# Optimization experiments

Hardware: AMD Instinct MI355X
Metric: run time of the kernel (lower is better)

The kernel has to match this reference:

```python
import jax, jax.numpy as jnp
import numpy as np

Z_DIM = 256
HID = 1024
VOCAB = 512
SEQ_LEN = 32 * 16  # subsequence_length * num_subsequences
BATCH = 64


def setup_inputs() -> dict:
    key = jax.random.key(0)
    ks = jax.random.split(key, 12)
    s = lambda *d: 1.0 / np.sqrt(d[-1])
    return {
        "z": jax.random.normal(ks[0], (BATCH, Z_DIM), jnp.float32),
        "fc_w": jax.random.uniform(ks[1], (HID, Z_DIM), jnp.float32, -s(Z_DIM), s(Z_DIM)),
        "fc_b": jnp.zeros((HID,), jnp.float32),
        "w_ih0": jax.random.uniform(ks[2], (4 * HID, VOCAB), jnp.float32, -s(HID), s(HID)),
        "w_hh0": jax.random.uniform(ks[3], (4 * HID, HID), jnp.float32, -s(HID), s(HID)),
        "b_ih0": jax.random.uniform(ks[4], (4 * HID,), jnp.float32, -s(HID), s(HID)),
        "b_hh0": jax.random.uniform(ks[5], (4 * HID,), jnp.float32, -s(HID), s(HID)),
        "w_ih1": jax.random.uniform(ks[6], (4 * HID, HID), jnp.float32, -s(HID), s(HID)),
        "w_hh1": jax.random.uniform(ks[7], (4 * HID, HID), jnp.float32, -s(HID), s(HID)),
        "b_ih1": jax.random.uniform(ks[8], (4 * HID,), jnp.float32, -s(HID), s(HID)),
        "b_hh1": jax.random.uniform(ks[9], (4 * HID,), jnp.float32, -s(HID), s(HID)),
        "out_w": jax.random.uniform(ks[10], (VOCAB, HID), jnp.float32, -s(HID), s(HID)),
        "out_b": jnp.zeros((VOCAB,), jnp.float32),
    }


def _lstm_cell(x, h, c, w_ih, w_hh, b):
    # PyTorch gate order: i, f, g, o
    gates = x @ w_ih.T + h @ w_hh.T + b  # [B, 4H]
    i, f, g, o = jnp.split(gates, 4, axis=-1)
    c_new = jax.nn.sigmoid(f) * c + jax.nn.sigmoid(i) * jnp.tanh(g)
    h_new = jax.nn.sigmoid(o) * jnp.tanh(c_new)
    return h_new, c_new


def reference(z, fc_w, fc_b, w_ih0, w_hh0, b_ih0, b_hh0,
              w_ih1, w_hh1, b_ih1, b_hh1, out_w, out_b):
    batch = z.shape[0]
    h_init = jnp.tanh(z @ fc_w.T + fc_b)  # [B, H], repeated for both layers
    h0 = h_init
    h1 = h_init
    c0 = jnp.zeros_like(h_init)
    c1 = jnp.zeros_like(h_init)
    x0 = jnp.zeros((batch, VOCAB), z.dtype)
    b0 = b_ih0 + b_hh0
    b1 = b_ih1 + b_hh1

    def step(carry, _):
        x, h0, c0, h1, c1 = carry
        h0, c0 = _lstm_cell(x, h0, c0, w_ih0, w_hh0, b0)
        h1, c1 = _lstm_cell(h0, h1, c1, w_ih1, w_hh1, b1)
        logits = h1 @ out_w.T + out_b  # [B, V]
        x_next = jax.nn.softmax(logits, axis=-1)
        return (x_next, h0, c0, h1, c1), logits

    _, logits_seq = jax.lax.scan(step, (x0, h0, c0, h1, c1), None, length=SEQ_LEN)
    # [T, B, V] -> [B, T, 1, V] (torch.stack of [B,1,V] slices along dim=1)
    return jnp.transpose(logits_seq, (1, 0, 2))[:, :, None, :]
```

## Files before the change

### kernel.cpp

```cpp
#include <hip/hip_runtime.h>
#include <hip/hip_cooperative_groups.h>
#include <math.h>

namespace cg = cooperative_groups;

#define Z_DIM   256
#define HID     1024
#define VOCAB   512
#define SEQ_LEN 512
#define BATCH   64
#define NBLK    256
#define NTHR    256
#define CHUNK   128

#define WS_EXPT   0
#define WS_RCPS   32768
#define WS_H0A    32832
#define WS_H0B    98368
#define WS_H1A    163904
#define WS_H1B    229440
#define WS_C0     294976
#define WS_C1     360512
#define WS_B0     426048
#define WS_B1     430144

__device__ __forceinline__ float sigm(float x) { return 1.f / (1.f + expf(-x)); }

__device__ __forceinline__ void phaseK(
    const float* __restrict__ w, int K,
    const float* __restrict__ src, int nc,
    int ju, int widx, int lane, int tid,
    float* __restrict__ sA, float* __restrict__ sW,
    float& gi, float& gf, float& gg, float& go)
{
    const int r  = lane >> 4;
    const int wc = (lane & 15) << 3;
    float4 a0, a1, a2, a3, a4, a5, a6, a7, vw0, vw1;

    auto pre = [&](int c) {
        const float4* g4 = (const float4*)(src + (size_t)(c * CHUNK) * 64);
        a0 = g4[tid];        a1 = g4[tid + 256];
        a2 = g4[tid + 512];  a3 = g4[tid + 768];
        a4 = g4[tid + 1024]; a5 = g4[tid + 1280];
        a6 = g4[tid + 1536]; a7 = g4[tid + 1792];
        const float* wp = w + (size_t)(r * HID + ju) * K + c * CHUNK + wc;
        vw0 = *(const float4*)wp;
        vw1 = *(const float4*)(wp + 4);
    };

    pre(0);
    for (int c = 0; c < nc; ++c) {
        __syncthreads();
        {
            float4* dA = (float4*)sA;
            dA[tid]        = a0; dA[tid + 256]  = a1;
            dA[tid + 512]  = a2; dA[tid + 768]  = a3;
            dA[tid + 1024] = a4; dA[tid + 1280] = a5;
            dA[tid + 1536] = a6; dA[tid + 1792] = a7;
            float* wd = sW + (widx * 4 + r) * CHUNK + wc;
            *(float4*)wd       = vw0;
            *(float4*)(wd + 4) = vw1;
        }
        __syncthreads();
        if (c + 1 < nc) pre(c + 1);
        const float* As = sA + lane;
        const float* Wr = sW + widx * 4 * CHUNK;
#pragma unroll
        for (int q = 0; q < CHUNK / 4; ++q) {
            const float4 wi = *(const float4*)&Wr[4 * q];
            const float4 wf = *(const float4*)&Wr[CHUNK + 4 * q];
            const float4 wg = *(const float4*)&Wr[2 * CHUNK + 4 * q];
            const float4 wo = *(const float4*)&Wr[3 * CHUNK + 4 * q];
            const float x0 = As[(q << 8)];
            const float x1 = As[(q << 8) + 64];
            const float x2 = As[(q << 8) + 128];
            const float x3 = As[(q << 8) + 192];
            gi = fmaf(wi.x, x0, fmaf(wi.y, x1, fmaf(wi.z, x2, fmaf(wi.w, x3, gi))));
            gf = fmaf(wf.x, x0, fmaf(wf.y, x1, fmaf(wf.z, x2, fmaf(wf.w, x3, gf))));
            gg = fmaf(wg.x, x0, fmaf(wg.y, x1, fmaf(wg.z, x2, fmaf(wg.w, x3, gg))));
            go = fmaf(wo.x, x0, fmaf(wo.y, x1, fmaf(wo.z, x2, fmaf(wo.w, x3, go))));
        }
    }
}

__global__ __launch_bounds__(NTHR) void lstm_persistent(
    const float* __restrict__ z,     const float* __restrict__ fc_w,
    const float* __restrict__ fc_b,  const float* __restrict__ w_ih0,
    const float* __restrict__ w_hh0, const float* __restrict__ b_ih0,
    const float* __restrict__ b_hh0, const float* __restrict__ w_ih1,
    const float* __restrict__ w_hh1, const float* __restrict__ b_ih1,
    const float* __restrict__ b_hh1, const float* __restrict__ out_w,
    const float* __restrict__ out_b, float* __restrict__ out,
    float* __restrict__ ws)
{
    cg::grid_group grid = cg::this_grid();
    const int tid  = threadIdx.x;
    const int lane = tid & 63;
    const int widx = tid >> 6;
    const int ju   = blockIdx.x * 4 + widx;

    float* expT = ws + WS_EXPT;
    float* rcpS = ws + WS_RCPS;
    float* h0A  = ws + WS_H0A;
    float* h0B  = ws + WS_H0B;
    float* h1A  = ws + WS_H1A;
    float* h1B  = ws + WS_H1B;
    float* c0T  = ws + WS_C0;
    float* c1T  = ws + WS_C1;
    float* b0   = ws + WS_B0;
    float* b1   = ws + WS_B1;

    __shared__ float sA[64 * CHUNK];
    __shared__ float sW[16 * CHUNK];
    __shared__ float h1s[HID];
    __shared__ float sred[8];

    {
        const int gtid = blockIdx.x * NTHR + tid;
        if (gtid < 4096)        b0[gtid] = b_ih0[gtid] + b_hh0[gtid];
        else if (gtid < 8192) { const int n = gtid - 4096; b1[n] = b_ih1[n] + b_hh1[n]; }
        if (gtid < 32768) expT[gtid] = 0.f;
        if (gtid < 64)    rcpS[gtid] = 1.f;
        const float4* wr = (const float4*)(fc_w + (size_t)ju * Z_DIM);
        const float4* zr = (const float4*)(z + (size_t)lane * Z_DIM);
        float acc = 0.f;
#pragma unroll 4
        for (int k4 = 0; k4 < Z_DIM / 4; ++k4) {
            const float4 a = wr[k4];
            const float4 x = zr[k4];
            acc = fmaf(a.x, x.x, fmaf(a.y, x.y, fmaf(a.z, x.z, fmaf(a.w, x.w, acc))));
        }
        const float h = tanhf(acc + fc_b[ju]);
        const int ci = (ju << 6) + lane;
        h0A[ci] = h;
        h1A[ci] = h;
        c0T[ci] = 0.f;
        c1T[ci] = 0.f;
    }
    grid.sync();

    for (int t = 0; t < SEQ_LEN; ++t) {
        const int par = t & 1;
        const float* h0_r = par ? h0B : h0A;
        float*       h0_w = par ? h0A : h0B;
        const float* h1_r = par ? h1B : h1A;
        float*       h1_w = par ? h1A : h1B;

        {
            float xi = 0.f, xf = 0.f, xg = 0.f, xo = 0.f;
            phaseK(w_ih0, VOCAB, expT, 4, ju, widx, lane, tid, sA, sW, xi, xf, xg, xo);
            const float rs = rcpS[lane];
            float gi = fmaf(xi, rs, b0[ju]);
            float gf = fmaf(xf, rs, b0[HID + ju]);
            float gg = fmaf(xg, rs, b0[2 * HID + ju]);
            float go = fmaf(xo, rs, b0[3 * HID + ju]);
            phaseK(w_hh0, HID, h0_r, 8, ju, widx, lane, tid, sA, sW, gi, gf, gg, go);
            const float i_ = sigm(gi), f_ = sigm(gf), g_ = tanhf(gg), o_ = sigm(go);
            const int ci = (ju << 6) + lane;
            const float cn = fmaf(f_, c0T[ci], i_ * g_);
            c0T[ci]  = cn;
            h0_w[ci] = o_ * tanhf(cn);
        }
        grid.sync();

        {
            float gi = b1[ju], gf = b1[HID + ju], gg = b1[2 * HID + ju], go = b1[3 * HID + ju];
            phaseK(w_ih1, HID, h0_w, 8, ju, widx, lane, tid, sA, sW, gi, gf, gg, go);
            phaseK(w_hh1, HID, h1_r, 8, ju, widx, lane, tid, sA, sW, gi, gf, gg, go);
            const float i_ = sigm(gi), f_ = sigm(gf), g_ = tanhf(gg), o_ = sigm(go);
            const int ci = (ju << 6) + lane;
            const float cn = fmaf(f_, c1T[ci], i_ * g_);
            c1T[ci]  = cn;
            h1_w[ci] = o_ * tanhf(cn);
        }
        grid.sync();

        if (blockIdx.x < BATCH) {
            const int b = blockIdx.x;
#pragma unroll
            for (int i = 0; i < 4; ++i) {
                const int k = tid + i * 256;
                h1s[k] = h1_w[(size_t)k * 64 + b];
            }
            __syncthreads();
            const int v0 = tid, v1 = tid + 256;
            float l0 = 0.f, l1 = 0.f;
            const float4* r0 = (const float4*)(out_w + (size_t)v0 * HID);
            const float4* r1 = (const float4*)(out_w + (size_t)v1 * HID);
#pragma unroll 4
            for (int k4 = 0; k4 < HID / 4; ++k4) {
                const float4 h = *(const float4*)&h1s[k4 << 2];
                const float4 a0 = r0[k4];
                const float4 a1 = r1[k4];
                l0 = fmaf(a0.x, h.x, l0); l1 = fmaf(a1.x, h.x, l1);
                l0 = fmaf(a0.y, h.y, l0); l1 = fmaf(a1.y, h.y, l1);
                l0 = fmaf(a0.z, h.z, l0); l1 = fmaf(a1.z, h.z, l1);
                l0 = fmaf(a0.w, h.w, l0); l1 = fmaf(a1.w, h.w, l1);
            }
            l0 += out_b[v0];
            l1 += out_b[v1];
            const size_t obase = ((size_t)b * SEQ_LEN + t) * VOCAB;
            out[obase + v0] = l0;
            out[obase + v1] = l1;
            float m = fmaxf(l0, l1);
#pragma unroll
            for (int off = 32; off; off >>= 1) m = fmaxf(m, __shfl_xor(m, off));
            if (lane == 0) sred[widx] = m;
            __syncthreads();
            const float M = fmaxf(fmaxf(sred[0], sred[1]), fmaxf(sred[2], sred[3]));
            const float e0 = expf(l0 - M);
            const float e1 = expf(l1 - M);
            float s = e0 + e1;
#pragma unroll
            for (int off = 32; off; off >>= 1) s += __shfl_xor(s, off);
            if (lane == 0) sred[4 + widx] = s;
            __syncthreads();
            expT[(size_t)v0 * 64 + b] = e0;
            expT[(size_t)v1 * 64 + b] = e1;
            if (tid == 0) rcpS[b] = 1.f / (sred[4] + sred[5] + sred[6] + sred[7]);
        }
        grid.sync();
    }
}

extern "C" void kernel_launch(void* const* d_in, const int* in_sizes, int n_in,
                              void* d_out, int out_size, void* d_ws, size_t ws_size,
                              hipStream_t stream) {
    const float* z     = (const float*)d_in[0];
    const float* fc_w  = (const float*)d_in[1];
    const float* fc_b  = (const float*)d_in[2];
    const float* w_ih0 = (const float*)d_in[3];
    const float* w_hh0 = (const float*)d_in[4];
    const float* b_ih0 = (const float*)d_in[5];
    const float* b_hh0 = (const float*)d_in[6];
    const float* w_ih1 = (const float*)d_in[7];
    const float* w_hh1 = (const float*)d_in[8];
    const float* b_ih1 = (const float*)d_in[9];
    const float* b_hh1 = (const float*)d_in[10];
    const float* out_w = (const float*)d_in[11];
    const float* out_b = (const float*)d_in[12];
    float* out = (float*)d_out;
    float* ws  = (float*)d_ws;

    void* args[] = { &z, &fc_w, &fc_b, &w_ih0, &w_hh0, &b_ih0, &b_hh0,
                     &w_ih1, &w_hh1, &b_ih1, &b_hh1, &out_w, &out_b, &out, &ws };
    hipLaunchCooperativeKernel((const void*)lstm_persistent,
                               dim3(NBLK), dim3(NTHR), args, 0, stream);
}
```

Baseline: 116.9 ms.

## Split gate GEMV K-dimension across 16 waves per block with shared-memory reduction

After: 226.5 ms. 93.7% more time.

```diff
diff --git a/kernel.cpp b/kernel.cpp
--- a/kernel.cpp
+++ b/kernel.cpp
@@ -10,42 +10,39 @@
 #define SEQ_LEN 512
 #define BATCH   64
 #define NBLK    256
-#define NTHR    256
+#define NTHR    1024
 #define CHUNK   128
 
-#define WS_EXPT   0
-#define WS_RCPS   32768
-#define WS_H0A    32832
-#define WS_H0B    98368
-#define WS_H1A    163904
-#define WS_H1B    229440
-#define WS_C0     294976
-#define WS_C1     360512
-#define WS_B0     426048
-#define WS_B1     430144
+#define WS_EXPT  0
+#define WS_H0A   32768
+#define WS_H0B   98304
+#define WS_H1A   163840
+#define WS_H1B   229376
+#define WS_C0    294912
+#define WS_C1    360448
+#define WS_B0    425984
+#define WS_B1    430080
 
 __device__ __forceinline__ float sigm(float x) { return 1.f / (1.f + expf(-x)); }
 
-__device__ __forceinline__ void phaseK(
+__device__ __forceinline__ void seg(
     const float* __restrict__ w, int K,
     const float* __restrict__ src, int nc,
-    int ju, int widx, int lane, int tid,
-    float* __restrict__ sA, float* __restrict__ sW,
-    float& gi, float& gf, float& gg, float& go)
+    int rbase, int u2, int s, int tid, int lane,
+    float* __restrict__ sA, float* __restrict__ sW, float* __restrict__ acc)
 {
-    const int r  = lane >> 4;
-    const int wc = (lane & 15) << 3;
-    float4 a0, a1, a2, a3, a4, a5, a6, a7, vw0, vw1;
+    float4 a0, a1, vw;
+    const int wrow = tid >> 5;
+    const int wcol = (tid & 31) << 2;
 
     auto pre = [&](int c) {
         const float4* g4 = (const float4*)(src + (size_t)(c * CHUNK) * 64);
-        a0 = g4[tid];        a1 = g4[tid + 256];
-        a2 = g4[tid + 512];  a3 = g4[tid + 768];
-        a4 = g4[tid + 1024]; a5 = g4[tid + 1280];
-        a6 = g4[tid + 1536]; a7 = g4[tid + 1792];
-        const float* wp = w + (size_t)(r * HID + ju) * K + c * CHUNK + wc;
-        vw0 = *(const float4*)wp;
-        vw1 = *(const float4*)(wp + 4);
+        a0 = g4[tid];
+        a1 = g4[tid + 1024];
+        if (tid < 512) {
+            const int g = wrow & 3, u = wrow >> 2;
+            vw = *(const float4*)(w + (size_t)(g * HID + rbase + u) * K + c * CHUNK + wcol);
+        }
     };
 
     pre(0);
@@ -53,37 +50,30 @@
         __syncthreads();
         {
             float4* dA = (float4*)sA;
-            dA[tid]        = a0; dA[tid + 256]  = a1;
-            dA[tid + 512]  = a2; dA[tid + 768]  = a3;
-            dA[tid + 1024] = a4; dA[tid + 1280] = a5;
-            dA[tid + 1536] = a6; dA[tid + 1792] = a7;
-            float* wd = sW + (widx * 4 + r) * CHUNK + wc;
-            *(float4*)wd       = vw0;
-            *(float4*)(wd + 4) = vw1;
+            dA[tid]        = a0;
+            dA[tid + 1024] = a1;
+            if (tid < 512) *(float4*)&sW[wrow * CHUNK + wcol] = vw;
         }
         __syncthreads();
         if (c + 1 < nc) pre(c + 1);
-        const float* As = sA + lane;
-        const float* Wr = sW + widx * 4 * CHUNK;
-#pragma unroll
-        for (int q = 0; q < CHUNK / 4; ++q) {
-            const float4 wi = *(const float4*)&Wr[4 * q];
-            const float4 wf = *(const float4*)&Wr[CHUNK + 4 * q];
-            const float4 wg = *(const float4*)&Wr[2 * CHUNK + 4 * q];
-            const float4 wo = *(const float4*)&Wr[3 * CHUNK + 4 * q];
-            const float x0 = As[(q << 8)];
-            const float x1 = As[(q << 8) + 64];
-            const float x2 = As[(q << 8) + 128];
-            const float x3 = As[(q << 8) + 192];
-            gi = fmaf(wi.x, x0, fmaf(wi.y, x1, fmaf(wi.z, x2, fmaf(wi.w, x3, gi))));
-            gf = fmaf(wf.x, x0, fmaf(wf.y, x1, fmaf(wf.z, x2, fmaf(wf.w, x3, gf))));
-            gg = fmaf(wg.x, x0, fmaf(wg.y, x1, fmaf(wg.z, x2, fmaf(wg.w, x3, gg))));
-            go = fmaf(wo.x, x0, fmaf(wo.y, x1, fmaf(wo.z, x2, fmaf(wo.w, x3, go))));
+        const float* As = sA + s * 16 * 64 + lane;
+        const float* Wr = sW + (u2 * 8) * CHUNK + s * 16;
+#pragma unroll
+        for (int q = 0; q < 4; ++q) {
+            const float x0 = As[(4 * q + 0) * 64];
+            const float x1 = As[(4 * q + 1) * 64];
+            const float x2 = As[(4 * q + 2) * 64];
+            const float x3 = As[(4 * q + 3) * 64];
+#pragma unroll
+            for (int j = 0; j < 8; ++j) {
+                const float4 wv = *(const float4*)&Wr[j * CHUNK + 4 * q];
+                acc[j] = fmaf(wv.x, x0, fmaf(wv.y, x1, fmaf(wv.z, x2, fmaf(wv.w, x3, acc[j]))));
+            }
         }
     }
 }
 
-__global__ __launch_bounds__(NTHR) void lstm_persistent(
+__global__ __launch_bounds__(NTHR, 4) void lstm_persistent(
     const float* __restrict__ z,     const float* __restrict__ fc_w,
     const float* __restrict__ fc_b,  const float* __restrict__ w_ih0,
     const float* __restrict__ w_hh0, const float* __restrict__ b_ih0,
@@ -97,45 +87,47 @@
     const int tid  = threadIdx.x;
     const int lane = tid & 63;
     const int widx = tid >> 6;
-    const int ju   = blockIdx.x * 4 + widx;
+    const int u2   = widx >> 3;
+    const int s    = widx & 7;
+    const int bid  = blockIdx.x;
+    const int rbase = bid * 4;
 
     float* expT = ws + WS_EXPT;
-    float* rcpS = ws + WS_RCPS;
     float* h0A  = ws + WS_H0A;
     float* h0B  = ws + WS_H0B;
     float* h1A  = ws + WS_H1A;
     float* h1B  = ws + WS_H1B;
     float* c0T  = ws + WS_C0;
     float* c1T  = ws + WS_C1;
-    float* b0   = ws + WS_B0;
-    float* b1   = ws + WS_B1;
+    float* b0v  = ws + WS_B0;
+    float* b1v  = ws + WS_B1;
 
     __shared__ float sA[64 * CHUNK];
     __shared__ float sW[16 * CHUNK];
+    __shared__ float sG[16 * 64];
     __shared__ float h1s[HID];
-    __shared__ float sred[8];
+    __shared__ float sred[16];
 
     {
-        const int gtid = blockIdx.x * NTHR + tid;
-        if (gtid < 4096)        b0[gtid] = b_ih0[gtid] + b_hh0[gtid];
-        else if (gtid < 8192) { const int n = gtid - 4096; b1[n] = b_ih1[n] + b_hh1[n]; }
+        const int gtid = bid * NTHR + tid;
+        if (gtid < 4096)        b0v[gtid] = b_ih0[gtid] + b_hh0[gtid];
+        else if (gtid < 8192) { const int n = gtid - 4096; b1v[n] = b_ih1[n] + b_hh1[n]; }
         if (gtid < 32768) expT[gtid] = 0.f;
-        if (gtid < 64)    rcpS[gtid] = 1.f;
-        const float4* wr = (const float4*)(fc_w + (size_t)ju * Z_DIM);
-        const float4* zr = (const float4*)(z + (size_t)lane * Z_DIM);
-        float acc = 0.f;
+        if (widx < 4) {
+            const int ju = rbase + widx;
+            const float4* wr = (const float4*)(fc_w + (size_t)ju * Z_DIM);
+            const float4* zr = (const float4*)(z + (size_t)lane * Z_DIM);
+            float acc = 0.f;
 #pragma unroll 4
-        for (int k4 = 0; k4 < Z_DIM / 4; ++k4) {
-            const float4 a = wr[k4];
-            const float4 x = zr[k4];
-            acc = fmaf(a.x, x.x, fmaf(a.y, x.y, fmaf(a.z, x.z, fmaf(a.w, x.w, acc))));
-        }
-        const float h = tanhf(acc + fc_b[ju]);
-        const int ci = (ju << 6) + lane;
-        h0A[ci] = h;
-        h1A[ci] = h;
-        c0T[ci] = 0.f;
-        c1T[ci] = 0.f;
+            for (int k4 = 0; k4 < Z_DIM / 4; ++k4) {
+                const float4 a = wr[k4];
+                const float4 x = zr[k4];
+                acc = fmaf(a.x, x.x, fmaf(a.y, x.y, fmaf(a.z, x.z, fmaf(a.w, x.w, acc))));
+            }
+            const float h = tanhf(acc + fc_b[ju]);
+            const int ci = (ju << 6) + lane;
+            h0A[ci] = h; h1A[ci] = h; c0T[ci] = 0.f; c1T[ci] = 0.f;
+        }
     }
     grid.sync();
 
@@ -147,77 +139,113 @@
         float*       h1_w = par ? h1A : h1B;
 
         {
-            float xi = 0.f, xf = 0.f, xg = 0.f, xo = 0.f;
-            phaseK(w_ih0, VOCAB, expT, 4, ju, widx, lane, tid, sA, sW, xi, xf, xg, xo);
-            const float rs = rcpS[lane];
-            float gi = fmaf(xi, rs, b0[ju]);
-            float gf = fmaf(xf, rs, b0[HID + ju]);
-            float gg = fmaf(xg, rs, b0[2 * HID + ju]);
-            float go = fmaf(xo, rs, b0[3 * HID + ju]);
-            phaseK(w_hh0, HID, h0_r, 8, ju, widx, lane, tid, sA, sW, gi, gf, gg, go);
-            const float i_ = sigm(gi), f_ = sigm(gf), g_ = tanhf(gg), o_ = sigm(go);
-            const int ci = (ju << 6) + lane;
-            const float cn = fmaf(f_, c0T[ci], i_ * g_);
-            c0T[ci]  = cn;
-            h0_w[ci] = o_ * tanhf(cn);
+            float acc[8] = {0, 0, 0, 0, 0, 0, 0, 0};
+            seg(w_ih0, VOCAB, expT, 4, rbase, u2, s, tid, lane, sA, sW, acc);
+            seg(w_hh0, HID, h0_r, 8, rbase, u2, s, tid, lane, sA, sW, acc);
+            __syncthreads();
+#pragma unroll
+            for (int j = 0; j < 8; ++j)
+                sA[(u2 * 8 + j) * 512 + s * 64 + lane] = acc[j];
+            __syncthreads();
+            {
+                const int r16 = tid >> 6, b = tid & 63;
+                const int g = r16 & 3, u = r16 >> 2;
+                float v = b0v[g * HID + rbase + u];
+#pragma unroll
+                for (int ss = 0; ss < 8; ++ss) v += sA[r16 * 512 + ss * 64 + b];
+                sG[r16 * 64 + b] = v;
+            }
+            __syncthreads();
+            if (tid < 256) {
+                const int u = tid >> 6, b = tid & 63;
+                const int ju = rbase + u;
+                const float i_ = sigm(sG[(u * 4 + 0) * 64 + b]);
+                const float f_ = sigm(sG[(u * 4 + 1) * 64 + b]);
+                const float g_ = tanhf(sG[(u * 4 + 2) * 64 + b]);
+                const float o_ = sigm(sG[(u * 4 + 3) * 64 + b]);
+                const int ci = (ju << 6) + b;
+                const float cn = fmaf(f_, c0T[ci], i_ * g_);
+                c0T[ci]  = cn;
+                h0_w[ci] = o_ * tanhf(cn);
+            }
         }
         grid.sync();
 
         {
-            float gi = b1[ju], gf = b1[HID + ju], gg = b1[2 * HID + ju], go = b1[3 * HID + ju];
-            phaseK(w_ih1, HID, h0_w, 8, ju, widx, lane, tid, sA, sW, gi, gf, gg, go);
-            phaseK(w_hh1, HID, h1_r, 8, ju, widx, lane, tid, sA, sW, gi, gf, gg, go);
-            const float i_ = sigm(gi), f_ = sigm(gf), g_ = tanhf(gg), o_ = sigm(go);
-            const int ci = (ju << 6) + lane;
-            const float cn = fmaf(f_, c1T[ci], i_ * g_);
-            c1T[ci]  = cn;
-            h1_w[ci] = o_ * tanhf(cn);
+            float acc[8] = {0, 0, 0, 0, 0, 0, 0, 0};
+            seg(w_ih1, HID, h0_w, 8, rbase, u2, s, tid, lane, sA, sW, acc);
+            seg(w_hh1, HID, h1_r, 8, rbase, u2, s, tid, lane, sA, sW, acc);
+            __syncthreads();
+#pragma unroll
+            for (int j = 0; j < 8; ++j)
+                sA[(u2 * 8 + j) * 512 + s * 64 + lane] = acc[j];
+            __syncthreads();
+            {
+                const int r16 = tid >> 6, b = tid & 63;
+                const int g = r16 & 3, u = r16 >> 2;
+                float v = b1v[g * HID + rbase + u];
+#pragma unroll
+                for (int ss = 0; ss < 8; ++ss) v += sA[r16 * 512 + ss * 64 + b];
+                sG[r16 * 64 + b] = v;
+            }
+            __syncthreads();
+            if (tid < 256) {
+                const int u = tid >> 6, b = tid & 63;
+                const int ju = rbase + u;
+                const float i_ = sigm(sG[(u * 4 + 0) * 64 + b]);
+                const float f_ = sigm(sG[(u * 4 + 1) * 64 + b]);
+                const float g_ = tanhf(sG[(u * 4 + 2) * 64 + b]);
+                const float o_ = sigm(sG[(u * 4 + 3) * 64 + b]);
+                const int ci = (ju << 6) + b;
+                const float cn = fmaf(f_, c1T[ci], i_ * g_);
+                c1T[ci]  = cn;
+                h1_w[ci] = o_ * tanhf(cn);
+            }
         }
         grid.sync();
 
-        if (blockIdx.x < BATCH) {
-            const int b = blockIdx.x;
-#pragma unroll
-            for (int i = 0; i < 4; ++i) {
-                const int k = tid + i * 256;
-                h1s[k] = h1_w[(size_t)k * 64 + b];
-            }
-            __syncthreads();
-            const int v0 = tid, v1 = tid + 256;
-            float l0 = 0.f, l1 = 0.f;
-            const float4* r0 = (const float4*)(out_w + (size_t)v0 * HID);
-            const float4* r1 = (const float4*)(out_w + (size_t)v1 * HID);
+        if (bid < BATCH) {
+            const int b = bid;
+            h1s[tid] = h1_w[(size_t)tid * 64 + b];
+            __syncthreads();
+            float l = 0.f, e = 0.f;
+            if (tid < 512) {
+                const int v = tid;
+                const float4* r0 = (const float4*)(out_w + (size_t)v * HID);
 #pragma unroll 4
-            for (int k4 = 0; k4 < HID / 4; ++k4) {
-                const float4 h = *(const float4*)&h1s[k4 << 2];
-                const float4 a0 = r0[k4];
-                const float4 a1 = r1[k4];
-                l0 = fmaf(a0.x, h.x, l0); l1 = fmaf(a1.x, h.x, l1);
-                l0 = fmaf(a0.y, h.y, l0); l1 = fmaf(a1.y, h.y, l1);
-                l0 = fmaf(a0.z, h.z, l0); l1 = fmaf(a1.z, h.z, l1);
-                l0 = fmaf(a0.w, h.w, l0); l1 = fmaf(a1.w, h.w, l1);
-            }
-            l0 += out_b[v0];
-            l1 += out_b[v1];
-            const size_t obase = ((size_t)b * SEQ_LEN + t) * VOCAB;
-            out[obase + v0] = l0;
-            out[obase + v1] = l1;
-            float m = fmaxf(l0, l1);
-#pragma unroll
-            for (int off = 32; off; off >>= 1) m = fmaxf(m, __shfl_xor(m, off));
-            if (lane == 0) sred[widx] = m;
-            __syncthreads();
-            const float M = fmaxf(fmaxf(sred[0], sred[1]), fmaxf(sred[2], sred[3]));
-            const float e0 = expf(l0 - M);
-            const float e1 = expf(l1 - M);
-            float s = e0 + e1;
-#pragma unroll
-            for (int off = 32; off; off >>= 1) s += __shfl_xor(s, off);
-            if (lane == 0) sred[4 + widx] = s;
-            __syncthreads();
-            expT[(size_t)v0 * 64 + b] = e0;
-            expT[(size_t)v1 * 64 + b] = e1;
-            if (tid == 0) rcpS[b] = 1.f / (sred[4] + sred[5] + sred[6] + sred[7]);
+                for (int k4 = 0; k4 < HID / 4; ++k4) {
+                    const float4 h = *(const float4*)&h1s[k4 << 2];
+                    const float4 a = r0[k4];
+                    l = fmaf(a.x, h.x, l);
+                    l = fmaf(a.y, h.y, l);
+                    l = fmaf(a.z, h.z, l);
+                    l = fmaf(a.w, h.w, l);
+                }
+                l += out_b[v];
+                out[((size_t)b * SEQ_LEN + t) * VOCAB + v] = l;
+                float m = l;
+#pragma unroll
+                for (int off = 32; off; off >>= 1) m = fmaxf(m, __shfl_xor(m, off));
+                if (lane == 0) sred[widx] = m;
+            }
+            __syncthreads();
+            if (tid < 512) {
+                float M = sred[0];
+#pragma unroll
+                for (int i = 1; i < 8; ++i) M = fmaxf(M, sred[i]);
+                e = expf(l - M);
+                float ssum = e;
+#pragma unroll
+                for (int off = 32; off; off >>= 1) ssum += __shfl_xor(ssum, off);
+                if (lane == 0) sred[8 + widx] = ssum;
+            }
+            __syncthreads();
+            if (tid < 512) {
+                float S = sred[8];
+#pragma unroll
+                for (int i = 1; i < 8; ++i) S += sred[8 + i];
+                expT[(size_t)tid * 64 + b] = e * (1.f / S);
+            }
         }
         grid.sync();
     }
@@ -226,6 +254,7 @@
 extern "C" void kernel_launch(void* const* d_in, const int* in_sizes, int n_in,
                               void* d_out, int out_size, void* d_ws, size_t ws_size,
                               hipStream_t stream) {
+    (void)in_sizes; (void)n_in; (void)out_size; (void)ws_size;
     const float* z     = (const float*)d_in[0];
     const float* fc_w  = (const float*)d_in[1];
     const float* fc_b  = (const float*)d_in[2];
```
